# Performance work log

Hardware: AMD Instinct MI355X
Metric: run time of the kernel (lower is better)

## Reference

```python
import jax, jax.numpy as jnp
import numpy as np

NB, NLOC, NALL, NNEI = 1, 4096, 6144, 64
N_EDGE, N_ANGLE, A_SEL = 262144, 409600, 10
N_DIM, E_DIM, A_DIM, AXIS = 128, 64, 32, 4
SEL_REDUCE = 10.0


def _lin_params(key, din, dout):
    k1, k2 = jax.random.split(key)
    W = jax.random.normal(k1, (din, dout), jnp.float32) / np.float32(np.sqrt(din))
    b = jax.random.normal(k2, (dout,), jnp.float32) * 0.01
    return W, b


def setup_inputs():
    key = jax.random.key(0)
    ks = jax.random.split(key, 20)
    inp = {}
    inp["node_ebd_ext"] = jax.random.normal(ks[0], (NB, NALL, N_DIM), jnp.float32)
    inp["edge_ebd"] = jax.random.normal(ks[1], (N_EDGE, E_DIM), jnp.float32)
    inp["h2"] = jax.random.normal(ks[2], (N_EDGE, 3), jnp.float32)
    inp["angle_ebd"] = jax.random.normal(ks[3], (N_ANGLE, A_DIM), jnp.float32)
    inp["nlist"] = jax.random.randint(ks[4], (NB, NLOC, NNEI), 0, NALL)
    inp["nlist_mask"] = jnp.ones((NB, NLOC, NNEI), jnp.bool_)
    inp["sw"] = jax.random.uniform(ks[5], (N_EDGE,), jnp.float32)
    inp["a_nlist"] = jax.random.randint(ks[6], (NB, NLOC, A_SEL), 0, NALL)
    inp["a_nlist_mask"] = jnp.ones((NB, NLOC, A_SEL), jnp.bool_)
    inp["a_sw"] = jax.random.uniform(ks[7], (N_ANGLE,), jnp.float32)
    n2e = jax.random.randint(ks[8], (N_EDGE,), 0, NB * NLOC)
    n_ext2e = jax.random.randint(ks[9], (N_EDGE,), 0, NB * NALL)
    inp["edge_index"] = jnp.stack([n2e, n_ext2e])
    n2a = jax.random.randint(ks[10], (N_ANGLE,), 0, NB * NLOC)
    eij2a = jax.random.randint(ks[11], (N_ANGLE,), 0, N_EDGE)
    eik2a = jax.random.randint(ks[12], (N_ANGLE,), 0, N_EDGE)
    inp["angle_index"] = jnp.stack([n2a, eij2a, eik2a])
    sym_dim = (N_DIM + E_DIM) * AXIS          # 768
    edge_info_dim = 2 * N_DIM + E_DIM         # 320
    angle_dim = A_DIM + N_DIM + 2 * E_DIM     # 288
    inp["W_node_self"], inp["b_node_self"] = _lin_params(ks[13], N_DIM, N_DIM)
    inp["W_node_sym"], inp["b_node_sym"] = _lin_params(ks[14], sym_dim, N_DIM)
    inp["W_node_edge"], inp["b_node_edge"] = _lin_params(ks[15], edge_info_dim, N_DIM)
    inp["W_edge_self"], inp["b_edge_self"] = _lin_params(ks[16], edge_info_dim, E_DIM)
    inp["W_edge_angle1"], inp["b_edge_angle1"] = _lin_params(ks[17], angle_dim, E_DIM)
    inp["W_edge_angle2"], inp["b_edge_angle2"] = _lin_params(ks[18], E_DIM, E_DIM)
    inp["W_angle_self"], inp["b_angle_self"] = _lin_params(ks[19], angle_dim, A_DIM)
    inp["n_res0"] = jnp.full((N_DIM,), 0.1, jnp.float32)
    inp["n_res1"] = jnp.full((N_DIM,), 0.1, jnp.float32)
    inp["n_res2"] = jnp.full((N_DIM,), 0.1, jnp.float32)
    inp["e_res0"] = jnp.full((E_DIM,), 0.1, jnp.float32)
    inp["e_res1"] = jnp.full((E_DIM,), 0.1, jnp.float32)
    inp["a_res0"] = jnp.full((A_DIM,), 0.1, jnp.float32)
    return inp


def reference(node_ebd_ext, edge_ebd, h2, angle_ebd, nlist, nlist_mask, sw,
              a_nlist, a_nlist_mask, a_sw, edge_index, angle_index,
              W_node_self, b_node_self, W_node_sym, b_node_sym,
              W_node_edge, b_node_edge, W_edge_self, b_edge_self,
              W_edge_angle1, b_edge_angle1, W_edge_angle2, b_edge_angle2,
              W_angle_self, b_angle_self,
              n_res0, n_res1, n_res2, e_res0, e_res1, a_res0):
    act = jax.nn.silu
    nb, nloc, nnei = nlist.shape
    n_dim = node_ebd_ext.shape[-1]
    n_edge = h2.shape[0]
    dyn_e_sel = nnei / SEL_REDUCE
    dyn_a_sel = a_nlist.shape[-1] / SEL_REDUCE
    node_ebd = node_ebd_ext[:, :nloc]
    n2e, n_ext2e = edge_index[0], edge_index[1]
    n2a, eij2a, eik2a = angle_index[0], angle_index[1], angle_index[2]
    nei_node_ebd = node_ebd_ext.reshape(-1, n_dim)[n_ext2e]  # [n_edge, n_dim]
    node_self = act(node_ebd @ W_node_self + b_node_self)

    def sym_op(flat_ebd):
        # symmetrization: outer(h2, sw*ebd) scattered to owners, then grrg
        d = flat_ebd.shape[-1]
        w = flat_ebd * sw[:, None]
        h2g2 = jax.ops.segment_sum(
            (h2[:, :, None] * w[:, None, :]).reshape(n_edge, 3 * d),
            n2e, num_segments=nb * nloc)
        h2g2 = h2g2.reshape(nb, nloc, 3, d) * (dyn_e_sel ** -0.5)
        m = h2g2[..., :AXIS]  # [nb, nloc, 3, axis]
        g = jnp.einsum('blxa,blxd->blad', m, h2g2) / 3.0
        return g.reshape(nb, nloc, AXIS * d)

    sym_edge = sym_op(edge_ebd)
    sym_node = sym_op(nei_node_ebd)
    node_sym = act(jnp.concatenate([sym_edge, sym_node], -1) @ W_node_sym + b_node_sym)
    node_i = node_ebd.reshape(-1, n_dim)[n2e]
    edge_info = jnp.concatenate([node_i, nei_node_ebd, edge_ebd], -1)  # [n_edge, 320]
    node_edge_update = act(edge_info @ W_node_edge + b_node_edge) * sw[:, None]
    node_edge_msg = jax.ops.segment_sum(node_edge_update, n2e, num_segments=nb * nloc).reshape(nb, nloc, -1) / dyn_e_sel
    n_updated = node_ebd + n_res0 * node_self + n_res1 * node_sym + n_res2 * node_edge_msg
    edge_self = act(edge_info @ W_edge_self + b_edge_self)
    node_for_angle = node_ebd.reshape(-1, n_dim)[n2a]
    edge_ik = edge_ebd[eik2a]
    edge_ij = edge_ebd[eij2a]
    angle_info = jnp.concatenate([angle_ebd, node_for_angle, edge_ik, edge_ij], -1)  # [n_angle, 288]
    edge_angle = act(angle_info @ W_edge_angle1 + b_edge_angle1)
    reduced = jax.ops.segment_sum(edge_angle * a_sw[:, None], eij2a, num_segments=n_edge) / (dyn_a_sel ** 0.5)
    edge_angle_msg = act(reduced @ W_edge_angle2 + b_edge_angle2)
    e_updated = edge_ebd + e_res0 * edge_self + e_res1 * edge_angle_msg
    angle_self = act(angle_info @ W_angle_self + b_angle_self)
    a_updated = angle_ebd + a_res0 * angle_self
    return (n_updated, e_updated, a_updated)
```

## Files before the change

### kernel.cpp

```cpp
#include <hip/hip_runtime.h>
#include <hip/hip_bf16.h>

#define NLOC_   4096
#define NALL_   6144
#define NEDGE_  262144
#define NANGLE_ 409600

typedef __bf16 bf16x8 __attribute__((ext_vector_type(8)));
typedef float  f32x4  __attribute__((ext_vector_type(4)));
typedef unsigned short u16;

__device__ __forceinline__ float silu_(float x){ return x / (1.0f + __expf(-x)); }

__device__ __forceinline__ u16 f2bu(float f){
    union { float f; unsigned u; } v; v.f = f;
    unsigned r = v.u + 0x7fffu + ((v.u >> 16) & 1u);
    return (u16)(r >> 16);
}
__device__ __forceinline__ float bu2f(u16 b){
    union { unsigned u; float f; } v; v.u = ((unsigned)b) << 16; return v.f;
}
__device__ __forceinline__ void st_bf16x4(u16* dst, float4 v){
    unsigned lo = (unsigned)f2bu(v.x) | ((unsigned)f2bu(v.y) << 16);
    unsigned hi = (unsigned)f2bu(v.z) | ((unsigned)f2bu(v.w) << 16);
    *reinterpret_cast<uint2*>(dst) = make_uint2(lo, hi);
}

__global__ __launch_bounds__(256) void k_mega_prep(
    const float* __restrict__ Wne, const float* __restrict__ Wes,
    const float* __restrict__ W1,  const float* __restrict__ WA,
    const float* __restrict__ W2,  const float* __restrict__ Wsym,
    const float* __restrict__ Wns,
    const float* __restrict__ node_ext, const float* __restrict__ edge_ebd,
    const float* __restrict__ angle_ebd,
    const int* __restrict__ n2e, const int* __restrict__ eij2a,
    u16* __restrict__ WTe, u16* __restrict__ WTa2, u16* __restrict__ WTaN,
    u16* __restrict__ WT2, u16* __restrict__ WsymT, u16* __restrict__ WnsT,
    u16* __restrict__ NB, u16* __restrict__ EB, u16* __restrict__ AB,
    int* __restrict__ cnt, int* __restrict__ cnt2)
{
    const int b = blockIdx.x, tid = threadIdx.x;
    if (b < 812) {
        int i = b*256 + tid;
        if (i < 61440) {
            int r = i/320, c = i - r*320;
            WTe[i] = f2bu(r < 128 ? Wne[c*128 + r] : Wes[c*64 + (r-128)]);
        } else if (i < 76800) {
            int j = i - 61440; int r = j/160, c2 = j - r*160;
            int k = (c2 < 32) ? c2 : c2 + 128;
            WTa2[j] = f2bu(r < 64 ? W1[k*64 + r] : WA[k*32 + (r-64)]);
        } else if (i < 89088) {
            int j = i - 76800; int r = j >> 7, c2 = j & 127;
            int k = c2 + 32;
            WTaN[j] = f2bu(r < 64 ? W1[k*64 + r] : WA[k*32 + (r-64)]);
        } else if (i < 93184) {
            int j = i - 89088; int r = j >> 6, c = j & 63;
            WT2[j] = f2bu(W2[c*64 + r]);
        } else if (i < 191488) {
            int j = i - 93184; int r = j/768, c = j - r*768;
            WsymT[j] = f2bu(Wsym[c*128 + r]);
        } else {
            int j = i - 191488; int r = j >> 7, c = j & 127;
            WnsT[j] = f2bu(Wns[c*128 + r]);
        }
    } else if (b < 1580) {
        int i = (b - 812)*256 + tid;
        float4 v = ((const float4*)node_ext)[i];
        st_bf16x4(&NB[(size_t)i*4], v);
    } else if (b < 3628) {
        for (int i = (b - 1580)*256 + tid; i < NEDGE_*64/4; i += 2048*256) {
            float4 v = ((const float4*)edge_ebd)[i];
            st_bf16x4(&EB[(size_t)i*4], v);
        }
    } else if (b < 5676) {
        for (int i = (b - 3628)*256 + tid; i < NANGLE_*32/4; i += 2048*256) {
            float4 v = ((const float4*)angle_ebd)[i];
            st_bf16x4(&AB[(size_t)i*4], v);
        }
    } else if (b < 6700) {
        int e = (b - 5676)*256 + tid;
        atomicAdd(&cnt[n2e[e]], 1);
    } else {
        int a = (b - 6700)*256 + tid;
        atomicAdd(&cnt2[eij2a[a]], 1);
    }
}

__global__ __launch_bounds__(256) void k_scan_misc(
    const int* __restrict__ cnt, int* __restrict__ off, int* __restrict__ cursor,
    const int* __restrict__ cnt2, int* __restrict__ bsum,
    const u16* __restrict__ NB, const u16* __restrict__ WTe,
    const u16* __restrict__ WTaN,
    float* __restrict__ nconst, float* __restrict__ nconstA)
{
    __shared__ __align__(16) u16 sN[64][136];
    int* wa = (int*)&sN[0][0];
    const int b = blockIdx.x, t = threadIdx.x;

    if (b == 0) {
        int v[16]; int s = 0;
        #pragma unroll
        for (int k = 0; k < 16; ++k) { v[k] = s; s += cnt[16*t + k]; }
        wa[t] = s;
        __syncthreads();
        for (int d = 1; d < 256; d <<= 1) {
            int x = wa[t];
            int y = (t >= d) ? wa[t-d] : 0;
            __syncthreads();
            wa[t] = x + y;
            __syncthreads();
        }
        int excl = (t == 0) ? 0 : wa[t-1];
        #pragma unroll
        for (int k = 0; k < 16; ++k) {
            off[16*t + k]    = excl + v[k];
            cursor[16*t + k] = excl + v[k];
        }
        if (t == 255) off[4096] = excl + s;
    } else if (b <= 256) {
        int bb = b - 1;
        int4 v = ((const int4*)cnt2)[bb*256 + t];
        wa[t] = v.x + v.y + v.z + v.w;
        __syncthreads();
        for (int d = 128; d > 0; d >>= 1) {
            if (t < d) wa[t] += wa[t+d];
            __syncthreads();
        }
        if (t == 0) bsum[bb] = wa[0];
    } else if (b <= 320) {
        const int e0 = (b - 257) * 64;
        #pragma unroll
        for (int f = t; f < 1024; f += 256) {
            int r = f >> 4, c = f & 15;
            *(uint4*)&sN[r][8*c] = ((const uint4*)&NB[(size_t)(e0 + r)*128])[c];
        }
        __syncthreads();
        const int w = t >> 6, l = t & 63;
        const int lr = l & 15, hq = l >> 4, lk = hq * 8;
        f32x4 acc[4][3] = {};
        #pragma unroll
        for (int kk = 0; kk < 4; ++kk) {
            bf16x8 a[4], bb[3];
            #pragma unroll
            for (int m = 0; m < 4; ++m)
                a[m] = *(const bf16x8*)&sN[16*m + lr][kk*32 + lk];
            #pragma unroll
            for (int nf = 0; nf < 3; ++nf)
                bb[nf] = *(const bf16x8*)&WTe[(size_t)(48*w + 16*nf + lr)*320 + kk*32 + lk];
            #pragma unroll
            for (int m = 0; m < 4; ++m)
                #pragma unroll
                for (int nf = 0; nf < 3; ++nf)
                    acc[m][nf] = __builtin_amdgcn_mfma_f32_16x16x32_bf16(a[m], bb[nf], acc[m][nf], 0, 0, 0);
        }
        #pragma unroll
        for (int nf = 0; nf < 3; ++nf) {
            int c = 48*w + 16*nf + lr;
            #pragma unroll
            for (int m = 0; m < 4; ++m)
                #pragma unroll
                for (int j = 0; j < 4; ++j) {
                    int r = 16*m + 4*hq + j;
                    nconst[(size_t)(e0 + r)*192 + c] = acc[m][nf][j];
                }
        }
    } else {
        const int n0 = (b - 321) * 64;
        #pragma unroll
        for (int f = t; f < 1024; f += 256) {
            int r = f >> 4, c = f & 15;
            *(uint4*)&sN[r][8*c] = ((const uint4*)&NB[(size_t)(n0 + r)*128])[c];
        }
        __syncthreads();
        const int w = t >> 6, l = t & 63;
        const int lr = l & 15, hq = l >> 4, lk = hq * 8;
        f32x4 acc[6] = {};
        #pragma unroll
        for (int kk = 0; kk < 4; ++kk) {
            bf16x8 a = *(const bf16x8*)&sN[16*w + lr][kk*32 + lk];
            #pragma unroll
            for (int nf = 0; nf < 6; ++nf) {
                bf16x8 bb = *(const bf16x8*)&WTaN[(size_t)(16*nf + lr)*128 + kk*32 + lk];
                acc[nf] = __builtin_amdgcn_mfma_f32_16x16x32_bf16(a, bb, acc[nf], 0, 0, 0);
            }
        }
        #pragma unroll
        for (int nf = 0; nf < 6; ++nf) {
            int c = 16*nf + lr;
            #pragma unroll
            for (int j = 0; j < 4; ++j) {
                int r = 16*w + 4*hq + j;
                nconstA[(size_t)(n0 + r)*96 + c] = acc[nf][j];
            }
        }
    }
}

__global__ void k_scan2b(const int* __restrict__ bsum, int* __restrict__ boff)
{
    __shared__ int wa[256];
    int t = threadIdx.x;
    wa[t] = bsum[t];
    __syncthreads();
    for (int d = 1; d < 256; d <<= 1) {
        int x = wa[t];
        int y = (t >= d) ? wa[t-d] : 0;
        __syncthreads();
        wa[t] = x + y;
        __syncthreads();
    }
    boff[t] = (t == 0) ? 0 : wa[t-1];
}

__global__ void k_scan2c(const int* __restrict__ cnt2, const int* __restrict__ boff,
                         int* __restrict__ off2, int* __restrict__ cursor2)
{
    __shared__ int wa[256];
    int b = blockIdx.x, t = threadIdx.x;
    int4 v = ((const int4*)cnt2)[b*256 + t];
    int s1 = v.x, s2 = s1 + v.y, s3 = s2 + v.z, s4 = s3 + v.w;
    wa[t] = s4;
    __syncthreads();
    for (int d = 1; d < 256; d <<= 1) {
        int x = wa[t];
        int y = (t >= d) ? wa[t-d] : 0;
        __syncthreads();
        wa[t] = x + y;
        __syncthreads();
    }
    int base = boff[b] + ((t == 0) ? 0 : wa[t-1]);
    int i = (b*256 + t)*4;
    off2[i]   = base;      cursor2[i]   = base;
    off2[i+1] = base + s1; cursor2[i+1] = base + s1;
    off2[i+2] = base + s2; cursor2[i+2] = base + s2;
    off2[i+3] = base + s3; cursor2[i+3] = base + s3;
    if (b == 255 && t == 255) off2[NEDGE_] = NANGLE_;
}

__global__ void k_fill2(const int* __restrict__ n2e, int* __restrict__ cursor,
                        int* __restrict__ csr,
                        const int* __restrict__ eij2a, int* __restrict__ cursor2,
                        int* __restrict__ csr2)
{
    int b = blockIdx.x;
    if (b < 1024) {
        int e = b*256 + threadIdx.x;
        int pos = atomicAdd(&cursor[n2e[e]], 1);
        csr[pos] = e;
    } else {
        int a = (b - 1024)*256 + threadIdx.x;
        int pos = atomicAdd(&cursor2[eij2a[a]], 1);
        csr2[pos] = a;
    }
}

__global__ __launch_bounds__(256, 4) void k_edge_flat(
    const u16* __restrict__ NB, const u16* __restrict__ EB,
    const float* __restrict__ h2, const float* __restrict__ sw,
    const int* __restrict__ n2e, const int* __restrict__ n_ext2e,
    const int* __restrict__ csr,
    const u16* __restrict__ WTe, const float* __restrict__ nconst,
    const float* __restrict__ bne, const float* __restrict__ bes,
    float* __restrict__ msg,
    float* __restrict__ h2g2_e, float* __restrict__ h2g2_n,
    u16* __restrict__ eselfO)
{
    __shared__ __align__(16) u16 sA[64][200];
    __shared__ float sH[4][576];
    __shared__ int   s_eid[64];
    __shared__ int   s_node[64];
    __shared__ int   s_g[64];
    __shared__ float s_sw[64];
    __shared__ float s_h2[64][3];
    __shared__ int   s_segstart[65];
    __shared__ int   s_nseg;

    const int tid = threadIdx.x;
    const int w  = tid >> 6, l = tid & 63;
    const int lr = l & 15, hq = l >> 4, lk = hq * 8;
    const int base = blockIdx.x * 64;

    if (tid < 64) {
        int e = csr[base + tid];
        s_eid[tid]  = e;
        s_node[tid] = n2e[e];
        s_g[tid]    = n_ext2e[e];
        s_sw[tid]   = sw[e];
        s_h2[tid][0] = h2[e*3];
        s_h2[tid][1] = h2[e*3+1];
        s_h2[tid][2] = h2[e*3+2];
    }
    __syncthreads();

    if (tid < 64) {
        bool flag = (tid == 0) || (s_node[tid] != s_node[tid-1]);
        unsigned long long mask = __ballot(flag);
        if (flag) {
            int sid = __popcll(mask & ((1ull << tid) - 1ull));
            s_segstart[sid] = tid;
        }
        if (tid == 0) {
            int ns = __popcll(mask);
            s_nseg = ns;
            s_segstart[ns] = 64;
        }
    }

    #pragma unroll
    for (int f = tid; f < 1024; f += 256) {
        int r = f >> 4, c = f & 15;
        *(uint4*)&sA[r][8*c] = ((const uint4*)&NB[(size_t)s_g[r]*128])[c];
    }
    #pragma unroll
    for (int f = tid; f < 512; f += 256) {
        int r = f >> 3, c = f & 7;
        *(uint4*)&sA[r][128 + 8*c] = ((const uint4*)&EB[(size_t)s_eid[r]*64])[c];
    }
    __syncthreads();

    float bias[3];
    int   cful[3];
    #pragma unroll
    for (int nf = 0; nf < 3; ++nf) {
        int c = 48*w + 16*nf + lr;
        cful[nf] = c;
        bias[nf] = (c < 128) ? bne[c] : bes[c-128];
    }

    f32x4 acc[4][3] = {};
    #pragma unroll
    for (int kk = 0; kk < 6; ++kk) {
        bf16x8 a[4], b[3];
        #pragma unroll
        for (int m = 0; m < 4; ++m)
            a[m] = *(const bf16x8*)&sA[16*m + lr][kk*32 + lk];
        #pragma unroll
        for (int nf = 0; nf < 3; ++nf)
            b[nf] = *(const bf16x8*)&WTe[(size_t)cful[nf]*320 + 128 + kk*32 + lk];
        #pragma unroll
        for (int m = 0; m < 4; ++m)
            #pragma unroll
            for (int nf = 0; nf < 3; ++nf)
                acc[m][nf] = __builtin_amdgcn_mfma_f32_16x16x32_bf16(a[m], b[nf], acc[m][nf], 0, 0, 0);
    }

    #pragma unroll
    for (int nf = 0; nf < 3; ++nf) {
        int c = cful[nf];
        if (c < 128) {
            #pragma unroll
            for (int m = 0; m < 4; ++m)
                #pragma unroll
                for (int j = 0; j < 4; ++j) {
                    int r = 16*m + 4*hq + j;
                    float ncv = nconst[(size_t)s_node[r]*192 + c];
                    acc[m][nf][j] = silu_(acc[m][nf][j] + ncv + bias[nf]) * s_sw[r];
                }
        } else {
            int c2 = c - 128;
            #pragma unroll
            for (int m = 0; m < 4; ++m)
                #pragma unroll
                for (int j = 0; j < 4; ++j) {
                    int r = 16*m + 4*hq + j;
                    float ncv = nconst[(size_t)s_node[r]*192 + c];
                    eselfO[(size_t)s_eid[r]*64 + c2] =
                        f2bu(silu_(acc[m][nf][j] + ncv + bias[nf]));
                }
        }
    }

    const int nseg = s_nseg;
    for (int s = 0; s < nseg; ++s) {
        int rs = s_segstart[s], re = s_segstart[s+1];
        int nd = s_node[rs];
        #pragma unroll
        for (int nf = 0; nf < 3; ++nf) {
            if (cful[nf] >= 128) continue;
            float v = 0.f;
            #pragma unroll
            for (int m = 0; m < 4; ++m)
                #pragma unroll
                for (int j = 0; j < 4; ++j) {
                    int r = 16*m + 4*hq + j;
                    v += (r >= rs && r < re) ? acc[m][nf][j] : 0.f;
                }
            v += __shfl_xor(v, 16);
            v += __shfl_xor(v, 32);
            if (hq == 0) atomicAdd(&msg[(size_t)nd*128 + cful[nf]], v);
        }
    }

    for (int s = 0; s < nseg; ++s) {
        int rs = s_segstart[s], re = s_segstart[s+1];
        int nd = s_node[rs];
        int lo = max(16*w, rs), hi = min(16*w + 16, re);
        float hacc[9] = {0.f,0.f,0.f,0.f,0.f,0.f,0.f,0.f,0.f};
        for (int r = lo; r < hi; ++r) {
            float swv = s_sw[r];
            float s0 = s_h2[r][0] * swv;
            float s1 = s_h2[r][1] * swv;
            float s2 = s_h2[r][2] * swv;
            float eb = bu2f(sA[r][128 + l]);
            float n0 = bu2f(sA[r][l]);
            float n1 = bu2f(sA[r][64 + l]);
            hacc[0] = fmaf(s0, eb, hacc[0]);
            hacc[1] = fmaf(s1, eb, hacc[1]);
            hacc[2] = fmaf(s2, eb, hacc[2]);
            hacc[3] = fmaf(s0, n0, hacc[3]);
            hacc[4] = fmaf(s0, n1, hacc[4]);
            hacc[5] = fmaf(s1, n0, hacc[5]);
            hacc[6] = fmaf(s1, n1, hacc[6]);
            hacc[7] = fmaf(s2, n0, hacc[7]);
            hacc[8] = fmaf(s2, n1, hacc[8]);
        }
        #pragma unroll
        for (int q = 0; q < 3; ++q) sH[w][q*64 + l] = hacc[q];
        #pragma unroll
        for (int q = 0; q < 6; ++q) sH[w][192 + q*64 + l] = hacc[3+q];
        __syncthreads();
        for (int i = tid; i < 576; i += 256) {
            float v = sH[0][i] + sH[1][i] + sH[2][i] + sH[3][i];
            if (i < 192) atomicAdd(&h2g2_e[(size_t)nd*192 + i], v);
            else         atomicAdd(&h2g2_n[(size_t)nd*384 + (i - 192)], v);
        }
        __syncthreads();
    }
}

__global__ __launch_bounds__(256) void k_angle_mfma(
    const u16* __restrict__ EB, const u16* __restrict__ AB,
    const float* __restrict__ a_sw,
    const int* __restrict__ n2a, const int* __restrict__ eij2a,
    const int* __restrict__ eik2a, const int* __restrict__ csr2,
    const u16* __restrict__ WTa2, const float* __restrict__ nconstA,
    const float* __restrict__ b1, const float* __restrict__ bA,
    const float* __restrict__ a_res0,
    u16* __restrict__ ea, float* __restrict__ a_out)
{
    __shared__ __align__(16) u16 sA[32][168];
    __shared__ __align__(16) u16 sEA[32][64];
    __shared__ int s_a[32], s_nd[32], s_ij[32], s_ik[32];
    __shared__ float s_asw[32];
    const int tid = threadIdx.x;
    const int p0 = blockIdx.x * 32;

    if (tid < 32) {
        int a = csr2[p0 + tid];
        s_a[tid]  = a;
        s_nd[tid] = n2a[a];
        s_ij[tid] = eij2a[a];
        s_ik[tid] = eik2a[a];
        s_asw[tid] = a_sw[a];
    }
    __syncthreads();

    if (tid < 128) {
        int r = tid >> 2, c = tid & 3;
        *(uint4*)&sA[r][8*c] = ((const uint4*)&AB[(size_t)s_a[r]*32])[c];
    }
    {
        int r = tid >> 3, c = tid & 7;
        *(uint4*)&sA[r][32 + 8*c] = ((const uint4*)&EB[(size_t)s_ik[r]*64])[c];
        *(uint4*)&sA[r][96 + 8*c] = ((const uint4*)&EB[(size_t)s_ij[r]*64])[c];
    }
    __syncthreads();

    const int w = tid >> 6, l = tid & 63;
    const int lr = l & 15, hq = l >> 4, lk = hq * 8;
    const int mrow  = (w & 1) * 16;
    const int nbase = (w >> 1) * 48;

    f32x4 acc[3] = {};
    #pragma unroll
    for (int kk = 0; kk < 5; ++kk) {
        bf16x8 a = *(const bf16x8*)&sA[mrow + lr][kk*32 + lk];
        #pragma unroll
        for (int nf = 0; nf < 3; ++nf) {
            bf16x8 b = *(const bf16x8*)&WTa2[(size_t)(nbase + 16*nf + lr)*160 + kk*32 + lk];
            acc[nf] = __builtin_amdgcn_mfma_f32_16x16x32_bf16(a, b, acc[nf], 0, 0, 0);
        }
    }

    #pragma unroll
    for (int nf = 0; nf < 3; ++nf) {
        int c = nbase + 16*nf + lr;
        if (c < 64) {
            float bb = b1[c];
            #pragma unroll
            for (int j = 0; j < 4; ++j) {
                int r = mrow + 4*hq + j;
                float nca = nconstA[(size_t)s_nd[r]*96 + c];
                sEA[r][c] = f2bu(silu_(acc[nf][j] + nca + bb) * s_asw[r]);
            }
        } else {
            int c2 = c - 64;
            float bb = bA[c2], rr = a_res0[c2];
            #pragma unroll
            for (int j = 0; j < 4; ++j) {
                int r = mrow + 4*hq + j;
                float nca = nconstA[(size_t)s_nd[r]*96 + c];
                a_out[(size_t)s_a[r]*32 + c2] =
                    bu2f(sA[r][c2]) + rr * silu_(acc[nf][j] + nca + bb);
            }
        }
    }
    __syncthreads();

    {
        int r = tid >> 3, c = tid & 7;
        *(uint4*)&ea[((size_t)(p0 + r))*64 + 8*c] = *(const uint4*)&sEA[r][8*c];
    }
}

__global__ __launch_bounds__(256) void k_fin(
    const u16* __restrict__ EB, const u16* __restrict__ eselfO,
    const u16* __restrict__ ea, const int* __restrict__ off2,
    const u16* __restrict__ WT2,
    const float* __restrict__ b2_, const float* __restrict__ er0,
    const float* __restrict__ er1,
    float* __restrict__ e_out,
    const float* __restrict__ h2g2_e, const float* __restrict__ h2g2_n,
    u16* __restrict__ symcB)
{
    __shared__ __align__(16) u16 sR[64][72];
    __shared__ __align__(16) u16 sE[64][72];
    __shared__ __align__(16) u16 sB[64][72];
    const int tid = threadIdx.x;
    const int blk = blockIdx.x;

    if (blk < 4096) {
        const int e0 = blk * 64;
        const int w = tid >> 6, l = tid & 63;

        #pragma unroll
        for (int f = tid; f < 512; f += 256) {
            int r = f >> 3, c = f & 7;
            *(uint4*)&sB[r][8*c] = ((const uint4*)&EB[(size_t)(e0 + r)*64])[c];
            *(uint4*)&sE[r][8*c] = ((const uint4*)&eselfO[(size_t)(e0 + r)*64])[c];
        }

        #pragma unroll
        for (int r16 = 0; r16 < 16; ++r16) {
            int r = w*16 + r16;
            int e = e0 + r;
            float s = 0.f;
            int jb = off2[e], je = off2[e+1];
            for (int j = jb; j < je; ++j)
                s += bu2f(ea[(size_t)j*64 + l]);
            sR[r][l] = f2bu(s);
        }
        __syncthreads();

        const int lr = l & 15, hq = l >> 4, lk = hq * 8;
        f32x4 acc[4] = {};
        #pragma unroll
        for (int kk = 0; kk < 2; ++kk) {
            bf16x8 b = *(const bf16x8*)&WT2[(size_t)(16*w + lr)*64 + kk*32 + lk];
            #pragma unroll
            for (int m = 0; m < 4; ++m) {
                bf16x8 a = *(const bf16x8*)&sR[16*m + lr][kk*32 + lk];
                acc[m] = __builtin_amdgcn_mfma_f32_16x16x32_bf16(a, b, acc[m], 0, 0, 0);
            }
        }
        int c = 16*w + lr;
        float bb = b2_[c], r0 = er0[c], r1 = er1[c];
        #pragma unroll
        for (int m = 0; m < 4; ++m)
            #pragma unroll
            for (int j = 0; j < 4; ++j) {
                int r = 16*m + 4*hq + j;
                size_t idx = (size_t)(e0 + r)*64 + c;
                e_out[idx] = bu2f(sB[r][c]) + r0 * bu2f(sE[r][c])
                           + r1 * silu_(acc[m][j] + bb);
            }
    } else {
        const int n = blk - 4096;
        float* he = (float*)&sR[0][0];
        float* hn = he + 192;
        for (int i = tid; i < 192; i += 256) he[i] = h2g2_e[(size_t)n*192 + i];
        for (int i = tid; i < 384; i += 256) hn[i] = h2g2_n[(size_t)n*384 + i];
        __syncthreads();
        const float SCALE = 1.0f / (6.4f * 3.0f);
        for (int i = tid; i < 768; i += 256) {
            float s;
            if (i < 256) {
                int a = i >> 6, j = i & 63;
                s = he[a]*he[j] + he[64+a]*he[64+j] + he[128+a]*he[128+j];
            } else {
                int i2 = i - 256;
                int a = i2 >> 7, j = i2 & 127;
                s = hn[a]*hn[j] + hn[128+a]*hn[128+j] + hn[256+a]*hn[256+j];
            }
            symcB[(size_t)n*768 + i] = f2bu(s * SCALE);
        }
    }
}

__global__ __launch_bounds__(256) void k_node_mfma(
    const u16* __restrict__ symcB, const u16* __restrict__ NB,
    const float* __restrict__ node_ext, const float* __restrict__ msg,
    const u16* __restrict__ WsymT, const u16* __restrict__ WnsT,
    const float* __restrict__ bns, const float* __restrict__ bsym,
    const float* __restrict__ nr0, const float* __restrict__ nr1,
    const float* __restrict__ nr2,
    float* __restrict__ n_out)
{
    __shared__ __align__(16) u16 sA[32][264];
    const int tid = threadIdx.x;
    const int n0 = blockIdx.x * 32;
    const int w = tid >> 6, l = tid & 63;
    const int lr = l & 15, hq = l >> 4, lk = hq * 8;

    f32x4 accY[2][2] = {};
    f32x4 accS[2][2] = {};

    for (int chunk = 0; chunk < 3; ++chunk) {
        __syncthreads();
        #pragma unroll
        for (int f = tid; f < 1024; f += 256) {
            int r = f >> 5, c = f & 31;
            *(uint4*)&sA[r][8*c] =
                ((const uint4*)&symcB[(size_t)(n0 + r)*768 + chunk*256])[c];
        }
        __syncthreads();
        #pragma unroll
        for (int kk = 0; kk < 8; ++kk) {
            bf16x8 a[2], b[2];
            #pragma unroll
            for (int m = 0; m < 2; ++m)
                a[m] = *(const bf16x8*)&sA[16*m + lr][kk*32 + lk];
            #pragma unroll
            for (int nf = 0; nf < 2; ++nf)
                b[nf] = *(const bf16x8*)&WsymT[(size_t)(32*w + 16*nf + lr)*768
                                               + chunk*256 + kk*32 + lk];
            #pragma unroll
            for (int m = 0; m < 2; ++m)
                #pragma unroll
                for (int nf = 0; nf < 2; ++nf)
                    accY[m][nf] = __builtin_amdgcn_mfma_f32_16x16x32_bf16(a[m], b[nf], accY[m][nf], 0, 0, 0);
        }
    }

    __syncthreads();
    #pragma unroll
    for (int f = tid; f < 512; f += 256) {
        int r = f >> 4, c = f & 15;
        *(uint4*)&sA[r][8*c] = ((const uint4*)&NB[(size_t)(n0 + r)*128])[c];
    }
    __syncthreads();
    #pragma unroll
    for (int kk = 0; kk < 4; ++kk) {
        bf16x8 a[2], b[2];
        #pragma unroll
        for (int m = 0; m < 2; ++m)
            a[m] = *(const bf16x8*)&sA[16*m + lr][kk*32 + lk];
        #pragma unroll
        for (int nf = 0; nf < 2; ++nf)
            b[nf] = *(const bf16x8*)&WnsT[(size_t)(32*w + 16*nf + lr)*128 + kk*32 + lk];
        #pragma unroll
        for (int m = 0; m < 2; ++m)
            #pragma unroll
            for (int nf = 0; nf < 2; ++nf)
                accS[m][nf] = __builtin_amdgcn_mfma_f32_16x16x32_bf16(a[m], b[nf], accS[m][nf], 0, 0, 0);
    }

    #pragma unroll
    for (int nf = 0; nf < 2; ++nf) {
        int c = 32*w + 16*nf + lr;
        float bS = bns[c], bY = bsym[c];
        float r0 = nr0[c], r1 = nr1[c], r2 = nr2[c];
        #pragma unroll
        for (int m = 0; m < 2; ++m)
            #pragma unroll
            for (int j = 0; j < 4; ++j) {
                int r = 16*m + 4*hq + j;
                size_t idx = (size_t)(n0 + r)*128 + c;
                float self_ = silu_(accS[m][nf][j] + bS);
                float sym_  = silu_(accY[m][nf][j] + bY);
                n_out[idx] = node_ext[idx] + r0*self_ + r1*sym_
                           + r2 * msg[idx] * (1.0f / 6.4f);
            }
    }
}

extern "C" void kernel_launch(void* const* d_in, const int* in_sizes, int n_in,
                              void* d_out, int out_size, void* d_ws, size_t ws_size,
                              hipStream_t stream)
{
    const float* node_ext  = (const float*)d_in[0];
    const float* edge_ebd  = (const float*)d_in[1];
    const float* h2        = (const float*)d_in[2];
    const float* angle_ebd = (const float*)d_in[3];
    const float* sw        = (const float*)d_in[6];
    const float* a_sw      = (const float*)d_in[9];
    const int*  edge_index  = (const int*)d_in[10];
    const int*  angle_index = (const int*)d_in[11];
    const int* n2e     = edge_index;
    const int* n_ext2e = edge_index + NEDGE_;
    const int* n2a     = angle_index;
    const int* eij2a   = angle_index + NANGLE_;
    const int* eik2a   = angle_index + 2*NANGLE_;

    const float* Wns  = (const float*)d_in[12];
    const float* bns  = (const float*)d_in[13];
    const float* Wsym = (const float*)d_in[14];
    const float* bsym = (const float*)d_in[15];
    const float* Wne  = (const float*)d_in[16];
    const float* bne  = (const float*)d_in[17];
    const float* Wes  = (const float*)d_in[18];
    const float* bes  = (const float*)d_in[19];
    const float* W1   = (const float*)d_in[20];
    const float* b1   = (const float*)d_in[21];
    const float* W2   = (const float*)d_in[22];
    const float* b2_  = (const float*)d_in[23];
    const float* WA   = (const float*)d_in[24];
    const float* bA   = (const float*)d_in[25];
    const float* nr0  = (const float*)d_in[26];
    const float* nr1  = (const float*)d_in[27];
    const float* nr2  = (const float*)d_in[28];
    const float* er0  = (const float*)d_in[29];
    const float* er1  = (const float*)d_in[30];
    const float* ar0  = (const float*)d_in[31];

    char* wsp = (char*)d_ws;
    u16*   ea      = (u16*)wsp;    wsp += (size_t)NANGLE_ * 64 * 2;
    u16*   EB      = (u16*)wsp;    wsp += (size_t)NEDGE_ * 64 * 2;
    u16*   NB      = (u16*)wsp;    wsp += (size_t)NALL_ * 128 * 2;
    u16*   AB      = (u16*)wsp;    wsp += (size_t)NANGLE_ * 32 * 2;
    u16*   eselfO  = (u16*)wsp;    wsp += (size_t)NEDGE_ * 64 * 2;
    u16*   symcB   = (u16*)wsp;    wsp += (size_t)NLOC_ * 768 * 2;
    int*   cnt     = (int*)wsp;    wsp += 4096 * 4;
    int*   cnt2    = (int*)wsp;    wsp += (size_t)NEDGE_ * 4;
    float* msg     = (float*)wsp;  wsp += (size_t)NLOC_ * 128 * 4;
    float* h2g2_e  = (float*)wsp;  wsp += (size_t)NLOC_ * 192 * 4;
    float* h2g2_n  = (float*)wsp;  wsp += (size_t)NLOC_ * 384 * 4;
    size_t zero_bytes = 4096*4 + (size_t)NEDGE_*4 + (size_t)NLOC_*128*4
                      + (size_t)NLOC_*192*4 + (size_t)NLOC_*384*4;
    int*   off     = (int*)wsp;    wsp += 4104 * 4;
    int*   cursor  = (int*)wsp;    wsp += 4096 * 4;
    int*   csr     = (int*)wsp;    wsp += (size_t)NEDGE_ * 4;
    int*   off2    = (int*)wsp;    wsp += ((size_t)NEDGE_ + 16) * 4;
    int*   cursor2 = (int*)wsp;    wsp += (size_t)NEDGE_ * 4;
    int*   bsum    = (int*)wsp;    wsp += 256 * 4;
    int*   boff    = (int*)wsp;    wsp += 256 * 4;
    int*   csr2    = (int*)wsp;    wsp += (size_t)NANGLE_ * 4;
    float* nconst  = (float*)wsp;  wsp += (size_t)NLOC_ * 192 * 4;
    float* nconstA = (float*)wsp;  wsp += (size_t)NLOC_ * 96 * 4;
    u16*   WTe     = (u16*)wsp;    wsp += 192 * 320 * 2;
    u16*   WTa2    = (u16*)wsp;    wsp += 96 * 160 * 2;
    u16*   WTaN    = (u16*)wsp;    wsp += 96 * 128 * 2;
    u16*   WT2     = (u16*)wsp;    wsp += 64 * 64 * 2;
    u16*   WsymT   = (u16*)wsp;    wsp += 128 * 768 * 2;
    u16*   WnsT    = (u16*)wsp;    wsp += 128 * 128 * 2;

    hipMemsetAsync(cnt, 0, zero_bytes, stream);

    float* n_out = (float*)d_out;
    float* e_out = n_out + (size_t)NLOC_ * 128;
    float* a_out = e_out + (size_t)NEDGE_ * 64;

    k_mega_prep <<<8300, 256, 0, stream>>>(Wne, Wes, W1, WA, W2, Wsym, Wns,
                                           node_ext, edge_ebd, angle_ebd,
                                           n2e, eij2a,
                                           WTe, WTa2, WTaN, WT2, WsymT, WnsT,
                                           NB, EB, AB, cnt, cnt2);
    k_scan_misc <<<385, 256, 0, stream>>>(cnt, off, cursor, cnt2, bsum,
                                          NB, WTe, WTaN, nconst, nconstA);
    k_scan2b <<<1, 256, 0, stream>>>(bsum, boff);
    k_scan2c <<<256, 256, 0, stream>>>(cnt2, boff, off2, cursor2);
    k_fill2  <<<2624, 256, 0, stream>>>(n2e, cursor, csr, eij2a, cursor2, csr2);

    k_edge_flat <<<NEDGE_/64, 256, 0, stream>>>(NB, EB, h2, sw, n2e, n_ext2e, csr,
                                                WTe, nconst, bne, bes,
                                                msg, h2g2_e, h2g2_n, eselfO);
    k_angle_mfma <<<NANGLE_/32, 256, 0, stream>>>(EB, AB, a_sw,
                                                  n2a, eij2a, eik2a, csr2,
                                                  WTa2, nconstA, b1, bA, ar0,
                                                  ea, a_out);
    k_fin <<<8192, 256, 0, stream>>>(EB, eselfO, ea, off2, WT2, b2_, er0, er1,
                                     e_out, h2g2_e, h2g2_n, symcB);
    k_node_mfma <<<NLOC_/32, 256, 0, stream>>>(symcB, NB, node_ext, msg,
                                               WsymT, WnsT, bns, bsym,
                                               nr0, nr1, nr2, n_out);
}
```

Measured before the change: 422.6 us.

## Drop angle bf16 pre-conversion, gather fp32 angles directly; shrink edge-kernel LDS

Removes the prep pass that converted angle_ebd to a bf16 copy. The angle kernel now reads fp32 rows directly and converts them when loading into LDS, which removes one full write and read of the angle array. The edge kernel replaces its per-wave 4x576 LDS partials with a single shared buffer filled by LDS atomics, and its launch-bounds occupancy hint goes from 4 to 5. The trade-off is more synchronisation per segment and LDS atomic contention, plus wider fp32 gathers in the angle kernel.

```diff
diff --git a/kernel.cpp b/kernel.cpp
--- a/kernel.cpp
+++ b/kernel.cpp
@@ -32,11 +32,10 @@
     const float* __restrict__ W2,  const float* __restrict__ Wsym,
     const float* __restrict__ Wns,
     const float* __restrict__ node_ext, const float* __restrict__ edge_ebd,
-    const float* __restrict__ angle_ebd,
     const int* __restrict__ n2e, const int* __restrict__ eij2a,
     u16* __restrict__ WTe, u16* __restrict__ WTa2, u16* __restrict__ WTaN,
     u16* __restrict__ WT2, u16* __restrict__ WsymT, u16* __restrict__ WnsT,
-    u16* __restrict__ NB, u16* __restrict__ EB, u16* __restrict__ AB,
+    u16* __restrict__ NB, u16* __restrict__ EB,
     int* __restrict__ cnt, int* __restrict__ cnt2)
 {
     const int b = blockIdx.x, tid = threadIdx.x;
@@ -72,16 +71,11 @@
             float4 v = ((const float4*)edge_ebd)[i];
             st_bf16x4(&EB[(size_t)i*4], v);
         }
-    } else if (b < 5676) {
-        for (int i = (b - 3628)*256 + tid; i < NANGLE_*32/4; i += 2048*256) {
-            float4 v = ((const float4*)angle_ebd)[i];
-            st_bf16x4(&AB[(size_t)i*4], v);
-        }
-    } else if (b < 6700) {
-        int e = (b - 5676)*256 + tid;
+    } else if (b < 4652) {
+        int e = (b - 3628)*256 + tid;
         atomicAdd(&cnt[n2e[e]], 1);
     } else {
-        int a = (b - 6700)*256 + tid;
+        int a = (b - 4652)*256 + tid;
         atomicAdd(&cnt2[eij2a[a]], 1);
     }
 }
@@ -254,7 +248,7 @@
     }
 }
 
-__global__ __launch_bounds__(256, 4) void k_edge_flat(
+__global__ __launch_bounds__(256, 5) void k_edge_flat(
     const u16* __restrict__ NB, const u16* __restrict__ EB,
     const float* __restrict__ h2, const float* __restrict__ sw,
     const int* __restrict__ n2e, const int* __restrict__ n_ext2e,
@@ -266,7 +260,7 @@
     u16* __restrict__ eselfO)
 {
     __shared__ __align__(16) u16 sA[64][200];
-    __shared__ float sH[4][576];
+    __shared__ float sHa[576];
     __shared__ int   s_eid[64];
     __shared__ int   s_node[64];
     __shared__ int   s_g[64];
@@ -395,41 +389,48 @@
         int rs = s_segstart[s], re = s_segstart[s+1];
         int nd = s_node[rs];
         int lo = max(16*w, rs), hi = min(16*w + 16, re);
-        float hacc[9] = {0.f,0.f,0.f,0.f,0.f,0.f,0.f,0.f,0.f};
-        for (int r = lo; r < hi; ++r) {
-            float swv = s_sw[r];
-            float s0 = s_h2[r][0] * swv;
-            float s1 = s_h2[r][1] * swv;
-            float s2 = s_h2[r][2] * swv;
-            float eb = bu2f(sA[r][128 + l]);
-            float n0 = bu2f(sA[r][l]);
-            float n1 = bu2f(sA[r][64 + l]);
-            hacc[0] = fmaf(s0, eb, hacc[0]);
-            hacc[1] = fmaf(s1, eb, hacc[1]);
-            hacc[2] = fmaf(s2, eb, hacc[2]);
-            hacc[3] = fmaf(s0, n0, hacc[3]);
-            hacc[4] = fmaf(s0, n1, hacc[4]);
-            hacc[5] = fmaf(s1, n0, hacc[5]);
-            hacc[6] = fmaf(s1, n1, hacc[6]);
-            hacc[7] = fmaf(s2, n0, hacc[7]);
-            hacc[8] = fmaf(s2, n1, hacc[8]);
-        }
-        #pragma unroll
-        for (int q = 0; q < 3; ++q) sH[w][q*64 + l] = hacc[q];
-        #pragma unroll
-        for (int q = 0; q < 6; ++q) sH[w][192 + q*64 + l] = hacc[3+q];
-        __syncthreads();
+
+        __syncthreads();
+        for (int i = tid; i < 576; i += 256) sHa[i] = 0.f;
+        __syncthreads();
+
+        if (lo < hi) {
+            float hacc[9] = {0.f,0.f,0.f,0.f,0.f,0.f,0.f,0.f,0.f};
+            for (int r = lo; r < hi; ++r) {
+                float swv = s_sw[r];
+                float s0 = s_h2[r][0] * swv;
+                float s1 = s_h2[r][1] * swv;
+                float s2 = s_h2[r][2] * swv;
+                float eb = bu2f(sA[r][128 + l]);
+                float n0 = bu2f(sA[r][l]);
+                float n1 = bu2f(sA[r][64 + l]);
+                hacc[0] = fmaf(s0, eb, hacc[0]);
+                hacc[1] = fmaf(s1, eb, hacc[1]);
+                hacc[2] = fmaf(s2, eb, hacc[2]);
+                hacc[3] = fmaf(s0, n0, hacc[3]);
+                hacc[4] = fmaf(s0, n1, hacc[4]);
+                hacc[5] = fmaf(s1, n0, hacc[5]);
+                hacc[6] = fmaf(s1, n1, hacc[6]);
+                hacc[7] = fmaf(s2, n0, hacc[7]);
+                hacc[8] = fmaf(s2, n1, hacc[8]);
+            }
+            #pragma unroll
+            for (int q = 0; q < 3; ++q) atomicAdd(&sHa[q*64 + l], hacc[q]);
+            #pragma unroll
+            for (int q = 0; q < 6; ++q) atomicAdd(&sHa[192 + q*64 + l], hacc[3+q]);
+        }
+        __syncthreads();
+
         for (int i = tid; i < 576; i += 256) {
-            float v = sH[0][i] + sH[1][i] + sH[2][i] + sH[3][i];
+            float v = sHa[i];
             if (i < 192) atomicAdd(&h2g2_e[(size_t)nd*192 + i], v);
             else         atomicAdd(&h2g2_n[(size_t)nd*384 + (i - 192)], v);
         }
-        __syncthreads();
     }
 }
 
 __global__ __launch_bounds__(256) void k_angle_mfma(
-    const u16* __restrict__ EB, const u16* __restrict__ AB,
+    const u16* __restrict__ EB, const float* __restrict__ angle_ebd,
     const float* __restrict__ a_sw,
     const int* __restrict__ n2a, const int* __restrict__ eij2a,
     const int* __restrict__ eik2a, const int* __restrict__ csr2,
@@ -455,9 +456,9 @@
     }
     __syncthreads();
 
-    if (tid < 128) {
-        int r = tid >> 2, c = tid & 3;
-        *(uint4*)&sA[r][8*c] = ((const uint4*)&AB[(size_t)s_a[r]*32])[c];
+    {
+        int r = tid >> 3, c = tid & 7;
+        st_bf16x4(&sA[r][4*c], ((const float4*)angle_ebd)[(size_t)s_a[r]*8 + c]);
     }
     {
         int r = tid >> 3, c = tid & 7;
@@ -727,7 +728,6 @@
     u16*   ea      = (u16*)wsp;    wsp += (size_t)NANGLE_ * 64 * 2;
     u16*   EB      = (u16*)wsp;    wsp += (size_t)NEDGE_ * 64 * 2;
     u16*   NB      = (u16*)wsp;    wsp += (size_t)NALL_ * 128 * 2;
-    u16*   AB      = (u16*)wsp;    wsp += (size_t)NANGLE_ * 32 * 2;
     u16*   eselfO  = (u16*)wsp;    wsp += (size_t)NEDGE_ * 64 * 2;
     u16*   symcB   = (u16*)wsp;    wsp += (size_t)NLOC_ * 768 * 2;
     int*   cnt     = (int*)wsp;    wsp += 4096 * 4;
@@ -760,11 +760,11 @@
     float* e_out = n_out + (size_t)NLOC_ * 128;
     float* a_out = e_out + (size_t)NEDGE_ * 64;
 
-    k_mega_prep <<<8300, 256, 0, stream>>>(Wne, Wes, W1, WA, W2, Wsym, Wns,
-                                           node_ext, edge_ebd, angle_ebd,
+    k_mega_prep <<<6252, 256, 0, stream>>>(Wne, Wes, W1, WA, W2, Wsym, Wns,
+                                           node_ext, edge_ebd,
                                            n2e, eij2a,
                                            WTe, WTa2, WTaN, WT2, WsymT, WnsT,
-                                           NB, EB, AB, cnt, cnt2);
+                                           NB, EB, cnt, cnt2);
     k_scan_misc <<<385, 256, 0, stream>>>(cnt, off, cursor, cnt2, bsum,
                                           NB, WTe, WTaN, nconst, nconstA);
     k_scan2b <<<1, 256, 0, stream>>>(bsum, boff);
@@ -774,7 +774,7 @@
     k_edge_flat <<<NEDGE_/64, 256, 0, stream>>>(NB, EB, h2, sw, n2e, n_ext2e, csr,
                                                 WTe, nconst, bne, bes,
                                                 msg, h2g2_e, h2g2_n, eselfO);
-    k_angle_mfma <<<NANGLE_/32, 256, 0, stream>>>(EB, AB, a_sw,
+    k_angle_mfma <<<NANGLE_/32, 256, 0, stream>>>(EB, angle_ebd, a_sw,
                                                   n2a, eij2a, eik2a, csr2,
                                                   WTa2, nconstA, b1, bA, ar0,
                                                   ea, a_out);
```

Result: slower. 482.3 us (+14.1%).
